# Kernel optimization log

Hardware: AMD Instinct MI355X
Metric: run time of the kernel (lower is better)

## Reference

```python
import jax, jax.numpy as jnp
import numpy as np

ATTN = 512
HIDDEN = 1024
NUM_GENES = 2048
NUM_GF = 4


def setup_inputs() -> dict:
    key = jax.random.key(0)
    ks = jax.random.split(key, 8)
    s = 0.1
    return {
        "genes": jax.random.normal(ks[0], (32, NUM_GENES, NUM_GF), dtype=jnp.float32),
        "smiles": jax.random.normal(ks[1], (32, 2048, HIDDEN), dtype=jnp.float32),
        "w_num_gene_features": s * jax.random.normal(ks[2], (NUM_GF,), dtype=jnp.float32),
        "w_genes": s * jax.random.normal(ks[3], (NUM_GENES, ATTN), dtype=jnp.float32),
        "b_genes": s * jax.random.normal(ks[4], (ATTN,), dtype=jnp.float32),
        "w_smiles": s * jax.random.normal(ks[5], (HIDDEN, ATTN), dtype=jnp.float32),
        "b_smiles": s * jax.random.normal(ks[6], (ATTN,), dtype=jnp.float32),
        "v": s * jax.random.normal(ks[7], (ATTN,), dtype=jnp.float32),
    }


def reference(genes, smiles, w_num_gene_features, w_genes, b_genes, w_smiles, b_smiles, v):
    # genes: [B, G, F] -> collapse feature axis: [B, G]
    genes_collapsed = jnp.einsum("bgf,f->bg", genes, w_num_gene_features)
    # gene context projection: [B, A]
    x = jnp.einsum("bg,ga->ba", genes_collapsed, w_genes) + b_genes
    # smiles projection: [B, T, A]
    y = jnp.einsum("bth,ha->bta", smiles, w_smiles) + b_smiles
    h = jnp.tanh(x[:, None, :] + y)  # [B, T, A]
    scores = jnp.einsum("bta,a->bt", h, v)  # [B, T]
    alphas = jax.nn.softmax(scores, axis=-1)  # [B, T]
    # attention-weighted sum over sequence: [B, H]
    return jnp.einsum("bth,bt->bh", smiles, alphas)
```

## Files before the change

### kernel.cpp

```cpp
#include <hip/hip_runtime.h>


typedef __bf16 bf16_t;
typedef bf16_t bf16x8 __attribute__((ext_vector_type(8)));
typedef float f32x16 __attribute__((ext_vector_type(16)));

__device__ __forceinline__ unsigned short f32_to_bf16_rne(float f) {
    unsigned int u = __builtin_bit_cast(unsigned int, f);
    u = (u + 0x7FFFu + ((u >> 16) & 1u)) >> 16;
    return (unsigned short)u;
}

__device__ __forceinline__ float fast_tanh(float x) {
    float cx = fminf(fmaxf(x, -30.f), 30.f);
    float e = __expf(2.f * cx);
    return (e - 1.f) / (e + 1.f);
}

__global__ void k0b_pack(const float* __restrict__ w, unsigned short* __restrict__ Bp) {
    int bid  = blockIdx.x;
    int lane = threadIdx.x;
    int atile2 = bid >> 6, gks16 = bid & 63;
    int col = atile2 * 32 + (lane & 31);
    int k0  = gks16 * 16 + (lane >> 5) * 8;
    unsigned short us[8];
#pragma unroll
    for (int e = 0; e < 8; ++e)
        us[e] = f32_to_bf16_rne(w[(size_t)(k0 + e) * 512 + col]);
    *(uint4*)(Bp + (size_t)bid * 512 + lane * 8) = *(const uint4*)us;
}

__global__ void k1a_gc(const float4* __restrict__ genes, const float* __restrict__ wngf,
                       float* __restrict__ gc) {
    int i = blockIdx.x * 256 + threadIdx.x;
    float4 g = genes[i];
    gc[i] = g.x * wngf[0] + g.y * wngf[1] + g.z * wngf[2] + g.w * wngf[3];
}

__global__ void k1b_x(const float* __restrict__ gc, const float* __restrict__ wg,
                      float* __restrict__ x) {
    __shared__ float gcl[256];
    int bx = blockIdx.x;
    int b = bx >> 4, ah = (bx >> 3) & 1, gch = bx & 7;
    int g0 = gch * 256;
    gcl[threadIdx.x] = gc[b * 2048 + g0 + threadIdx.x];
    __syncthreads();
    int a = ah * 256 + threadIdx.x;
    float s = 0.f;
#pragma unroll 8
    for (int g = 0; g < 256; ++g) s += gcl[g] * wg[(size_t)(g0 + g) * 512 + a];
    atomicAdd(&x[b * 512 + a], s);
}

__global__ __launch_bounds__(512, 4) void k2_scores(
    const float* __restrict__ smiles,
    const unsigned short* __restrict__ Bp,
    const float* __restrict__ xraw,
    const float* __restrict__ b_genes,
    const float* __restrict__ b_smiles,
    const float* __restrict__ v,
    float* __restrict__ scores)
{
    __shared__ char A_lds[2 * 64 * 256];
    const int tid  = threadIdx.x;
    const int wave = tid >> 6;
    const int lane = tid & 63;
    const int l31  = lane & 31;
    const int hi   = lane >> 5;
    const int gm0  = blockIdx.x * 64;
    const int bidx = gm0 >> 11;
    const int wbase = wave * 64;

    const unsigned short* bpp = Bp + (size_t)(wave * 2) * 64 * 512 + lane * 8;

    const int srow = tid >> 3;
    const float* sptr = smiles + (size_t)(gm0 + srow) * 1024 + (tid & 7) * 16;
    const int sswz = (srow & 15) << 4;
    char* wr0 = (char*)A_lds + srow * 256 + (((tid & 7) * 32) ^ sswz);
    char* wr1 = (char*)A_lds + srow * 256 + ((((tid & 7) * 32) + 16) ^ sswz);

    float4 st0, st1, st2, st3;

    f32x16 acc[2][2];
#pragma unroll
    for (int mt = 0; mt < 2; ++mt)
#pragma unroll
        for (int nt = 0; nt < 2; ++nt)
#pragma unroll
            for (int r = 0; r < 16; ++r)
                acc[mt][nt][r] = 0.f;

#define LOADREGS(kt)                                   \
    {   const float* p = sptr + (kt) * 128;            \
        st0 = *(const float4*)(p);                     \
        st1 = *(const float4*)(p + 4);                 \
        st2 = *(const float4*)(p + 8);                 \
        st3 = *(const float4*)(p + 12); }

#define CONVWRITE(buf)                                                     \
    {   union { unsigned short us[8]; uint4 u4; } pa, pb;                  \
        pa.us[0] = f32_to_bf16_rne(st0.x); pa.us[1] = f32_to_bf16_rne(st0.y); \
        pa.us[2] = f32_to_bf16_rne(st0.z); pa.us[3] = f32_to_bf16_rne(st0.w); \
        pa.us[4] = f32_to_bf16_rne(st1.x); pa.us[5] = f32_to_bf16_rne(st1.y); \
        pa.us[6] = f32_to_bf16_rne(st1.z); pa.us[7] = f32_to_bf16_rne(st1.w); \
        pb.us[0] = f32_to_bf16_rne(st2.x); pb.us[1] = f32_to_bf16_rne(st2.y); \
        pb.us[2] = f32_to_bf16_rne(st2.z); pb.us[3] = f32_to_bf16_rne(st2.w); \
        pb.us[4] = f32_to_bf16_rne(st3.x); pb.us[5] = f32_to_bf16_rne(st3.y); \
        pb.us[6] = f32_to_bf16_rne(st3.z); pb.us[7] = f32_to_bf16_rne(st3.w); \
        *(uint4*)(wr0 + (buf) * 16384) = pa.u4;                            \
        *(uint4*)(wr1 + (buf) * 16384) = pb.u4; }

#define COMPUTE(cur, kt)                                                        \
    _Pragma("unroll")                                                           \
    for (int ks = 0; ks < 8; ++ks) {                                            \
        bf16x8 af[2], bfb[2];                                                   \
        _Pragma("unroll")                                                       \
        for (int nt = 0; nt < 2; ++nt)                                          \
            bfb[nt] = *(const bf16x8*)(bpp + (size_t)(nt * 64 + (kt) * 8 + ks) * 512); \
        _Pragma("unroll")                                                       \
        for (int mt = 0; mt < 2; ++mt) {                                        \
            int row = mt * 32 + l31;                                            \
            int byteoff = (cur) * 16384 + row * 256 +                           \
                          ((ks * 32 + hi * 16) ^ ((row & 15) << 4));            \
            af[mt] = *(const bf16x8*)(A_lds + byteoff);                         \
        }                                                                       \
        __builtin_amdgcn_s_setprio(1);                                          \
        _Pragma("unroll")                                                       \
        for (int mt = 0; mt < 2; ++mt)                                          \
            _Pragma("unroll")                                                   \
            for (int nt = 0; nt < 2; ++nt)                                      \
                acc[mt][nt] = __builtin_amdgcn_mfma_f32_32x32x16_bf16(          \
                    af[mt], bfb[nt], acc[mt][nt], 0, 0, 0);                     \
        __builtin_amdgcn_s_setprio(0);                                          \
    }

    LOADREGS(0);
    CONVWRITE(0);
    __syncthreads();

    int cur = 0;
#pragma unroll 1
    for (int kt = 0; kt < 7; ++kt) {
        LOADREGS(kt + 1);
        COMPUTE(cur, kt);
        CONVWRITE(cur ^ 1);
        __syncthreads();
        cur ^= 1;
    }
    COMPUTE(cur, 7);

#undef LOADREGS
#undef CONVWRITE
#undef COMPUTE

    float xbv[2], vv[2];
#pragma unroll
    for (int nt = 0; nt < 2; ++nt) {
        int a = wbase + nt * 32 + l31;
        xbv[nt] = xraw[bidx * 512 + a] + b_genes[a] + b_smiles[a];
        vv[nt]  = v[a];
    }
#pragma unroll
    for (int mt = 0; mt < 2; ++mt) {
        float rs[16];
#pragma unroll
        for (int r = 0; r < 16; ++r) rs[r] = 0.f;
#pragma unroll
        for (int nt = 0; nt < 2; ++nt)
#pragma unroll
            for (int r = 0; r < 16; ++r)
                rs[r] += vv[nt] * fast_tanh(acc[mt][nt][r] + xbv[nt]);
#pragma unroll
        for (int r = 0; r < 16; ++r) {
            float s = rs[r];
            s += __shfl_xor(s, 1);
            s += __shfl_xor(s, 2);
            s += __shfl_xor(s, 4);
            s += __shfl_xor(s, 8);
            s += __shfl_xor(s, 16);
            rs[r] = s;
        }
        if (l31 == 0) {
#pragma unroll
            for (int r = 0; r < 16; ++r) {
                int row = (r & 3) + 8 * (r >> 2) + 4 * hi;
                atomicAdd(&scores[gm0 + mt * 32 + row], rs[r]);
            }
        }
    }
}

__global__ void k3_softmax(const float* __restrict__ scores, float* __restrict__ alphas) {
    __shared__ float redmax[4], redsum[4];
    int b = blockIdx.x, tid = threadIdx.x;
    int wave = tid >> 6;
    float sv[8];
    float mx = -1e30f;
#pragma unroll
    for (int i = 0; i < 8; ++i) {
        sv[i] = scores[b * 2048 + i * 256 + tid];
        mx = fmaxf(mx, sv[i]);
    }
#pragma unroll
    for (int m = 32; m >= 1; m >>= 1) mx = fmaxf(mx, __shfl_xor(mx, m));
    if ((tid & 63) == 0) redmax[wave] = mx;
    __syncthreads();
    mx = fmaxf(fmaxf(redmax[0], redmax[1]), fmaxf(redmax[2], redmax[3]));
    float sum = 0.f;
#pragma unroll
    for (int i = 0; i < 8; ++i) {
        sv[i] = __expf(sv[i] - mx);
        sum += sv[i];
    }
#pragma unroll
    for (int m = 32; m >= 1; m >>= 1) sum += __shfl_xor(sum, m);
    if ((tid & 63) == 0) redsum[wave] = sum;
    __syncthreads();
    sum = redsum[0] + redsum[1] + redsum[2] + redsum[3];
    float inv = 1.f / sum;
#pragma unroll
    for (int i = 0; i < 8; ++i) alphas[b * 2048 + i * 256 + tid] = sv[i] * inv;
}

__global__ void k4_out(const float* __restrict__ smiles,
                       const float* __restrict__ alphas,
                       float* __restrict__ out)
{
    int bx = blockIdx.x;
    int b  = bx >> 5;
    int tc = bx & 31;
    int h  = threadIdx.x * 4;
    const float* sb = smiles + ((size_t)b * 2048 + tc * 64) * 1024;
    const float* al = alphas + b * 2048 + tc * 64;
    float4 acc = {0.f, 0.f, 0.f, 0.f};
#pragma unroll 4
    for (int t = 0; t < 64; ++t) {
        float a = al[t];
        float4 sv = *(const float4*)(sb + (size_t)t * 1024 + h);
        acc.x += a * sv.x;
        acc.y += a * sv.y;
        acc.z += a * sv.z;
        acc.w += a * sv.w;
    }
    float* o = out + b * 1024 + h;
    atomicAdd(o + 0, acc.x);
    atomicAdd(o + 1, acc.y);
    atomicAdd(o + 2, acc.z);
    atomicAdd(o + 3, acc.w);
}

extern "C" void kernel_launch(void* const* d_in, const int* in_sizes, int n_in,
                              void* d_out, int out_size, void* d_ws, size_t ws_size,
                              hipStream_t stream) {
    const float* genes    = (const float*)d_in[0];
    const float* smiles   = (const float*)d_in[1];
    const float* w_ngf    = (const float*)d_in[2];
    const float* w_genes  = (const float*)d_in[3];
    const float* b_genes  = (const float*)d_in[4];
    const float* w_smiles = (const float*)d_in[5];
    const float* b_smiles = (const float*)d_in[6];
    const float* v        = (const float*)d_in[7];
    float* out = (float*)d_out;

    char* ws = (char*)d_ws;
    unsigned short* Bp = (unsigned short*)(ws);
    float* gc     = (float*)(ws + (1 << 20));
    float* x      = (float*)(ws + (1 << 20) + (256 << 10));
    float* scores = (float*)(ws + (1 << 20) + (320 << 10));
    float* alphas = (float*)(ws + (1 << 20) + (576 << 10));

    hipMemsetAsync(out, 0, (size_t)32 * 1024 * sizeof(float), stream);
    hipMemsetAsync(x, 0, (size_t)(64 + 256) * 1024, stream);

    k0b_pack<<<1024, 64, 0, stream>>>(w_smiles, Bp);
    k1a_gc<<<256, 256, 0, stream>>>((const float4*)genes, w_ngf, gc);
    k1b_x<<<512, 256, 0, stream>>>(gc, w_genes, x);
    k2_scores<<<1024, 512, 0, stream>>>(smiles, Bp, x, b_genes, b_smiles, v, scores);
    k3_softmax<<<32, 256, 0, stream>>>(scores, alphas);
    k4_out<<<1024, 256, 0, stream>>>(smiles, alphas, out);
}
```

Baseline: 182.9 us.

## Fuse scores, softmax and weighted sum into one kernel reusing the LDS-resident smiles tile

```diff
diff --git a/kernel.cpp b/kernel.cpp
--- a/kernel.cpp
+++ b/kernel.cpp
@@ -9,6 +9,11 @@
     unsigned int u = __builtin_bit_cast(unsigned int, f);
     u = (u + 0x7FFFu + ((u >> 16) & 1u)) >> 16;
     return (unsigned short)u;
+}
+
+__device__ __forceinline__ float bf16bits_to_f32(unsigned short u) {
+    unsigned int w = ((unsigned int)u) << 16;
+    return __builtin_bit_cast(float, w);
 }
 
 __device__ __forceinline__ float fast_tanh(float x) {
@@ -52,16 +57,20 @@
     atomicAdd(&x[b * 512 + a], s);
 }
 
-__global__ __launch_bounds__(512, 4) void k2_scores(
+__global__ __launch_bounds__(1024, 4) void k2_mega(
     const float* __restrict__ smiles,
     const unsigned short* __restrict__ Bp,
     const float* __restrict__ xraw,
     const float* __restrict__ b_genes,
     const float* __restrict__ b_smiles,
     const float* __restrict__ v,
-    float* __restrict__ scores)
+    float* __restrict__ Zparts,
+    float* __restrict__ Oparts)
 {
-    __shared__ char A_lds[2 * 64 * 256];
+    __shared__ char A_lds[64 * 2048];
+    __shared__ float score_lds[64];
+    __shared__ float eS_lds[64];
+
     const int tid  = threadIdx.x;
     const int wave = tid >> 6;
     const int lane = tid & 63;
@@ -69,68 +78,55 @@
     const int hi   = lane >> 5;
     const int gm0  = blockIdx.x * 64;
     const int bidx = gm0 >> 11;
-    const int wbase = wave * 64;
-
-    const unsigned short* bpp = Bp + (size_t)(wave * 2) * 64 * 512 + lane * 8;
-
-    const int srow = tid >> 3;
-    const float* sptr = smiles + (size_t)(gm0 + srow) * 1024 + (tid & 7) * 16;
+
+    const unsigned short* bpp = Bp + (size_t)wave * 64 * 512 + lane * 8;
+
+    const int srow = tid >> 4;
+    const int sg   = tid & 15;
+    const float* sptr = smiles + (size_t)(gm0 + srow) * 1024 + sg * 8;
+    char* wrp = A_lds + srow * 2048;
     const int sswz = (srow & 15) << 4;
-    char* wr0 = (char*)A_lds + srow * 256 + (((tid & 7) * 32) ^ sswz);
-    char* wr1 = (char*)A_lds + srow * 256 + ((((tid & 7) * 32) + 16) ^ sswz);
-
-    float4 st0, st1, st2, st3;
-
-    f32x16 acc[2][2];
+
+    if (tid < 64) score_lds[tid] = 0.f;
+
+    float4 st0, st1;
+    f32x16 acc[2];
 #pragma unroll
     for (int mt = 0; mt < 2; ++mt)
 #pragma unroll
-        for (int nt = 0; nt < 2; ++nt)
-#pragma unroll
-            for (int r = 0; r < 16; ++r)
-                acc[mt][nt][r] = 0.f;
+        for (int r = 0; r < 16; ++r)
+            acc[mt][r] = 0.f;
 
 #define LOADREGS(kt)                                   \
     {   const float* p = sptr + (kt) * 128;            \
         st0 = *(const float4*)(p);                     \
-        st1 = *(const float4*)(p + 4);                 \
-        st2 = *(const float4*)(p + 8);                 \
-        st3 = *(const float4*)(p + 12); }
-
-#define CONVWRITE(buf)                                                     \
-    {   union { unsigned short us[8]; uint4 u4; } pa, pb;                  \
+        st1 = *(const float4*)(p + 4); }
+
+#define CONVWRITE(kt)                                                         \
+    {   union { unsigned short us[8]; uint4 u4; } pa;                         \
         pa.us[0] = f32_to_bf16_rne(st0.x); pa.us[1] = f32_to_bf16_rne(st0.y); \
         pa.us[2] = f32_to_bf16_rne(st0.z); pa.us[3] = f32_to_bf16_rne(st0.w); \
         pa.us[4] = f32_to_bf16_rne(st1.x); pa.us[5] = f32_to_bf16_rne(st1.y); \
         pa.us[6] = f32_to_bf16_rne(st1.z); pa.us[7] = f32_to_bf16_rne(st1.w); \
-        pb.us[0] = f32_to_bf16_rne(st2.x); pb.us[1] = f32_to_bf16_rne(st2.y); \
-        pb.us[2] = f32_to_bf16_rne(st2.z); pb.us[3] = f32_to_bf16_rne(st2.w); \
-        pb.us[4] = f32_to_bf16_rne(st3.x); pb.us[5] = f32_to_bf16_rne(st3.y); \
-        pb.us[6] = f32_to_bf16_rne(st3.z); pb.us[7] = f32_to_bf16_rne(st3.w); \
-        *(uint4*)(wr0 + (buf) * 16384) = pa.u4;                            \
-        *(uint4*)(wr1 + (buf) * 16384) = pb.u4; }
-
-#define COMPUTE(cur, kt)                                                        \
+        *(uint4*)(wrp + (((kt) * 256 + sg * 16) ^ sswz)) = pa.u4; }
+
+#define COMPUTE4(kt, ks0)                                                       \
     _Pragma("unroll")                                                           \
-    for (int ks = 0; ks < 8; ++ks) {                                            \
-        bf16x8 af[2], bfb[2];                                                   \
-        _Pragma("unroll")                                                       \
-        for (int nt = 0; nt < 2; ++nt)                                          \
-            bfb[nt] = *(const bf16x8*)(bpp + (size_t)(nt * 64 + (kt) * 8 + ks) * 512); \
+    for (int ks = (ks0); ks < (ks0) + 4; ++ks) {                                \
+        bf16x8 af[2], bfb;                                                      \
+        bfb = *(const bf16x8*)(bpp + (size_t)((kt) * 8 + ks) * 512);            \
         _Pragma("unroll")                                                       \
         for (int mt = 0; mt < 2; ++mt) {                                        \
             int row = mt * 32 + l31;                                            \
-            int byteoff = (cur) * 16384 + row * 256 +                           \
-                          ((ks * 32 + hi * 16) ^ ((row & 15) << 4));            \
+            int byteoff = row * 2048 +                                          \
+                (((kt) * 256 + ks * 32 + hi * 16) ^ ((row & 15) << 4));         \
             af[mt] = *(const bf16x8*)(A_lds + byteoff);                         \
         }                                                                       \
         __builtin_amdgcn_s_setprio(1);                                          \
         _Pragma("unroll")                                                       \
         for (int mt = 0; mt < 2; ++mt)                                          \
-            _Pragma("unroll")                                                   \
-            for (int nt = 0; nt < 2; ++nt)                                      \
-                acc[mt][nt] = __builtin_amdgcn_mfma_f32_32x32x16_bf16(          \
-                    af[mt], bfb[nt], acc[mt][nt], 0, 0, 0);                     \
+            acc[mt] = __builtin_amdgcn_mfma_f32_32x32x16_bf16(                  \
+                af[mt], bfb, acc[mt], 0, 0, 0);                                 \
         __builtin_amdgcn_s_setprio(0);                                          \
     }
 
@@ -138,115 +134,88 @@
     CONVWRITE(0);
     __syncthreads();
 
-    int cur = 0;
 #pragma unroll 1
-    for (int kt = 0; kt < 7; ++kt) {
-        LOADREGS(kt + 1);
-        COMPUTE(cur, kt);
-        CONVWRITE(cur ^ 1);
-        __syncthreads();
-        cur ^= 1;
-    }
-    COMPUTE(cur, 7);
+    for (int kt = 0; kt < 8; ++kt) {
+        if (kt < 7) LOADREGS(kt + 1);
+        COMPUTE4(kt, 0);
+        if (kt < 7) CONVWRITE(kt + 1);
+        COMPUTE4(kt, 4);
+        if (kt < 7) __syncthreads();
+    }
 
 #undef LOADREGS
 #undef CONVWRITE
-#undef COMPUTE
-
-    float xbv[2], vv[2];
-#pragma unroll
-    for (int nt = 0; nt < 2; ++nt) {
-        int a = wbase + nt * 32 + l31;
-        xbv[nt] = xraw[bidx * 512 + a] + b_genes[a] + b_smiles[a];
-        vv[nt]  = v[a];
-    }
-#pragma unroll
-    for (int mt = 0; mt < 2; ++mt) {
-        float rs[16];
-#pragma unroll
-        for (int r = 0; r < 16; ++r) rs[r] = 0.f;
-#pragma unroll
-        for (int nt = 0; nt < 2; ++nt)
+#undef COMPUTE4
+
+    {
+        int a = wave * 32 + l31;
+        float xbv = xraw[bidx * 512 + a] + b_genes[a] + b_smiles[a];
+        float vv  = v[a];
+        float prs[2][16];
+#pragma unroll
+        for (int mt = 0; mt < 2; ++mt)
 #pragma unroll
             for (int r = 0; r < 16; ++r)
-                rs[r] += vv[nt] * fast_tanh(acc[mt][nt][r] + xbv[nt]);
-#pragma unroll
-        for (int r = 0; r < 16; ++r) {
-            float s = rs[r];
-            s += __shfl_xor(s, 1);
-            s += __shfl_xor(s, 2);
-            s += __shfl_xor(s, 4);
-            s += __shfl_xor(s, 8);
-            s += __shfl_xor(s, 16);
-            rs[r] = s;
+                prs[mt][r] = vv * fast_tanh(acc[mt][r] + xbv);
+#pragma unroll
+        for (int mt = 0; mt < 2; ++mt)
+#pragma unroll
+            for (int r = 0; r < 16; ++r) {
+                float s = prs[mt][r];
+                s += __shfl_xor(s, 1);
+                s += __shfl_xor(s, 2);
+                s += __shfl_xor(s, 4);
+                s += __shfl_xor(s, 8);
+                s += __shfl_xor(s, 16);
+                prs[mt][r] = s;
+            }
+        if (l31 == 0) {
+#pragma unroll
+            for (int mt = 0; mt < 2; ++mt)
+#pragma unroll
+                for (int r = 0; r < 16; ++r) {
+                    int row = (r & 3) + 8 * (r >> 2) + 4 * hi;
+                    atomicAdd(&score_lds[mt * 32 + row], prs[mt][r]);
+                }
         }
-        if (l31 == 0) {
-#pragma unroll
-            for (int r = 0; r < 16; ++r) {
-                int row = (r & 3) + 8 * (r >> 2) + 4 * hi;
-                atomicAdd(&scores[gm0 + mt * 32 + row], rs[r]);
-            }
+    }
+    __syncthreads();
+
+    if (tid < 64) {
+        float e = __expf(score_lds[tid]);
+        eS_lds[tid] = e;
+        float s = e;
+#pragma unroll
+        for (int m = 1; m <= 32; m <<= 1) s += __shfl_xor(s, m);
+        if (tid == 0) Zparts[blockIdx.x] = s;
+    }
+    __syncthreads();
+
+    {
+        float accO = 0.f;
+#pragma unroll 8
+        for (int r = 0; r < 64; ++r) {
+            unsigned short u = *(const unsigned short*)(
+                A_lds + r * 2048 + ((tid * 2) ^ ((r & 15) << 4)));
+            accO += eS_lds[r] * bf16bits_to_f32(u);
         }
-    }
-}
-
-__global__ void k3_softmax(const float* __restrict__ scores, float* __restrict__ alphas) {
-    __shared__ float redmax[4], redsum[4];
-    int b = blockIdx.x, tid = threadIdx.x;
-    int wave = tid >> 6;
-    float sv[8];
-    float mx = -1e30f;
-#pragma unroll
-    for (int i = 0; i < 8; ++i) {
-        sv[i] = scores[b * 2048 + i * 256 + tid];
-        mx = fmaxf(mx, sv[i]);
-    }
-#pragma unroll
-    for (int m = 32; m >= 1; m >>= 1) mx = fmaxf(mx, __shfl_xor(mx, m));
-    if ((tid & 63) == 0) redmax[wave] = mx;
-    __syncthreads();
-    mx = fmaxf(fmaxf(redmax[0], redmax[1]), fmaxf(redmax[2], redmax[3]));
-    float sum = 0.f;
-#pragma unroll
-    for (int i = 0; i < 8; ++i) {
-        sv[i] = __expf(sv[i] - mx);
-        sum += sv[i];
-    }
-#pragma unroll
-    for (int m = 32; m >= 1; m >>= 1) sum += __shfl_xor(sum, m);
-    if ((tid & 63) == 0) redsum[wave] = sum;
-    __syncthreads();
-    sum = redsum[0] + redsum[1] + redsum[2] + redsum[3];
-    float inv = 1.f / sum;
-#pragma unroll
-    for (int i = 0; i < 8; ++i) alphas[b * 2048 + i * 256 + tid] = sv[i] * inv;
-}
-
-__global__ void k4_out(const float* __restrict__ smiles,
-                       const float* __restrict__ alphas,
-                       float* __restrict__ out)
+        Oparts[(size_t)blockIdx.x * 1024 + tid] = accO;
+    }
+}
+
+__global__ void k5_norm(const float* __restrict__ Zparts,
+                        const float* __restrict__ Oparts,
+                        float* __restrict__ out)
 {
-    int bx = blockIdx.x;
-    int b  = bx >> 5;
-    int tc = bx & 31;
-    int h  = threadIdx.x * 4;
-    const float* sb = smiles + ((size_t)b * 2048 + tc * 64) * 1024;
-    const float* al = alphas + b * 2048 + tc * 64;
-    float4 acc = {0.f, 0.f, 0.f, 0.f};
-#pragma unroll 4
-    for (int t = 0; t < 64; ++t) {
-        float a = al[t];
-        float4 sv = *(const float4*)(sb + (size_t)t * 1024 + h);
-        acc.x += a * sv.x;
-        acc.y += a * sv.y;
-        acc.z += a * sv.z;
-        acc.w += a * sv.w;
-    }
-    float* o = out + b * 1024 + h;
-    atomicAdd(o + 0, acc.x);
-    atomicAdd(o + 1, acc.y);
-    atomicAdd(o + 2, acc.z);
-    atomicAdd(o + 3, acc.w);
+    int i = blockIdx.x * 256 + threadIdx.x;
+    int b = i >> 10, h = i & 1023;
+    float z = 0.f, o = 0.f;
+#pragma unroll 8
+    for (int c = 0; c < 32; ++c) {
+        z += Zparts[b * 32 + c];
+        o += Oparts[(size_t)(b * 32 + c) * 1024 + h];
+    }
+    out[i] = o / z;
 }
 
 extern "C" void kernel_launch(void* const* d_in, const int* in_sizes, int n_in,
@@ -266,16 +235,15 @@
     unsigned short* Bp = (unsigned short*)(ws);
     float* gc     = (float*)(ws + (1 << 20));
     float* x      = (float*)(ws + (1 << 20) + (256 << 10));
-    float* scores = (float*)(ws + (1 << 20) + (320 << 10));
-    float* alphas = (float*)(ws + (1 << 20) + (576 << 10));
-
-    hipMemsetAsync(out, 0, (size_t)32 * 1024 * sizeof(float), stream);
-    hipMemsetAsync(x, 0, (size_t)(64 + 256) * 1024, stream);
+    float* Zparts = (float*)(ws + (1 << 20) + (320 << 10));
+    float* Oparts = (float*)(ws + (1 << 20) + (384 << 10));
+
+    hipMemsetAsync(x, 0, (size_t)64 * 1024, stream);
 
     k0b_pack<<<1024, 64, 0, stream>>>(w_smiles, Bp);
     k1a_gc<<<256, 256, 0, stream>>>((const float4*)genes, w_ngf, gc);
     k1b_x<<<512, 256, 0, stream>>>(gc, w_genes, x);
-    k2_scores<<<1024, 512, 0, stream>>>(smiles, Bp, x, b_genes, b_smiles, v, scores);
-    k3_softmax<<<32, 256, 0, stream>>>(scores, alphas);
-    k4_out<<<1024, 256, 0, stream>>>(smiles, alphas, out);
-}
+    k2_mega<<<1024, 1024, 0, stream>>>(smiles, Bp, x, b_genes, b_smiles, v,
+                                       Zparts, Oparts);
+    k5_norm<<<128, 256, 0, stream>>>(Zparts, Oparts, out);
+}
```

New measurement: 188.9 us. +3.3%, slower.
